# Kernel optimization log

Hardware: AMD Instinct MI355X
Metric: run time of the kernel (lower is better)

Reference implementation:

```python
import jax, jax.numpy as jnp
import numpy as np

B, C, H, W = 4, 256, 128, 128
D = 256            # attention hidden_dim (== C, so no output_proj)
HID = 1024         # mlp hidden = int(C * 4.0)
EPS = 1e-5


def setup_inputs() -> dict:
    key = jax.random.key(0)
    ks = jax.random.split(key, 16)
    s = 0.02
    return {
        "x": jax.random.normal(ks[0], (B, C, H, W), jnp.float32),
        "wq": jax.random.normal(ks[1], (C, D), jnp.float32) * s,
        "bq": jnp.zeros((D,), jnp.float32),
        "wk": jax.random.normal(ks[2], (C, D), jnp.float32) * s,
        "bk": jnp.zeros((D,), jnp.float32),
        "wv": jax.random.normal(ks[3], (C, D), jnp.float32) * s,
        "bv": jnp.zeros((D,), jnp.float32),
        "ln1_g": jnp.ones((C,), jnp.float32),
        "ln1_b": jnp.zeros((C,), jnp.float32),
        "ln2_g": jnp.ones((C,), jnp.float32),
        "ln2_b": jnp.zeros((C,), jnp.float32),
        "fc1_w": jax.random.normal(ks[4], (C, HID), jnp.float32) * s,
        "fc1_b": jnp.zeros((HID,), jnp.float32),
        "fc2_w": jax.random.normal(ks[5], (HID, C), jnp.float32) * s,
        "fc2_b": jnp.zeros((C,), jnp.float32),
    }


def _layernorm(x, g, b):
    m = jnp.mean(x, axis=-1, keepdims=True)
    v = jnp.mean(jnp.square(x - m), axis=-1, keepdims=True)
    return (x - m) * jax.lax.rsqrt(v + EPS) * g + b


def _neighborhoods(t):
    # t: [B,H,W,D] -> [B,H,W,9,D] 3x3 neighborhoods, zero-padded at borders
    tp = jnp.pad(t, ((0, 0), (1, 1), (1, 1), (0, 0)))
    h, w = t.shape[1], t.shape[2]
    return jnp.stack(
        [tp[:, dy:dy + h, dx:dx + w, :] for dy in range(3) for dx in range(3)],
        axis=3,
    )


def _valid_mask(h, w):
    # [H,W,9] bool: which of the 9 neighbors are inside the grid
    ys = jnp.arange(h)[:, None] * jnp.ones((1, w), jnp.int32)
    xs = jnp.arange(w)[None, :] * jnp.ones((h, 1), jnp.int32)
    top, bot = ys > 0, ys < h - 1
    lef, rig = xs > 0, xs < w - 1
    ones = jnp.ones((h, w), bool)
    return jnp.stack(
        [top & lef, top, top & rig, lef, ones, rig, bot & lef, bot, bot & rig],
        axis=-1,
    )


def reference(x, wq, bq, wk, bk, wv, bv, ln1_g, ln1_b, ln2_g, ln2_b,
              fc1_w, fc1_b, fc2_w, fc2_b):
    b_, c_, h_, w_ = x.shape
    xc = jnp.transpose(x, (0, 2, 3, 1))                    # [B,H,W,C]
    n1 = _layernorm(xc, ln1_g, ln1_b)
    q = n1 @ wq + bq                                       # [B,H,W,D]
    k = n1 @ wk + bk
    v = n1 @ wv + bv
    kn = _neighborhoods(k)                                  # [B,H,W,9,D]
    vn = _neighborhoods(v)
    scores = jnp.einsum('bhwd,bhwnd->bhwn', q, kn) / jnp.sqrt(jnp.float32(q.shape[-1]))
    mask = _valid_mask(h_, w_)                               # [H,W,9]
    scores = jnp.where(mask, scores, jnp.float32(-1e9))
    weights = jax.nn.softmax(scores, axis=-1)
    attn = jnp.einsum('bhwn,bhwnd->bhwd', weights, vn)       # [B,H,W,D]
    x1 = xc + attn                                           # residual 1
    n2 = _layernorm(x1, ln2_g, ln2_b)
    mlp = jax.nn.gelu(n2 @ fc1_w + fc1_b, approximate=False) @ fc2_w + fc2_b
    out = x1 + mlp
    return jnp.transpose(out, (0, 3, 1, 2))                  # [B,C,H,W]
```

## Files before the change

kernel.cpp:

```cpp
#include <hip/hip_runtime.h>
#include <hip/hip_bf16.h>
#include <math.h>

#define NPIX  65536
#define CCH   256
#define HWSZ  16384
#define WIDTH 128
#define HID   1024

typedef unsigned short u16;
typedef __bf16 bf16x8 __attribute__((ext_vector_type(8)));
typedef float  floatx4 __attribute__((ext_vector_type(4)));

__device__ __forceinline__ float bf2f(u16 u) {
  union { unsigned int i; float f; } c; c.i = ((unsigned int)u) << 16; return c.f;
}
__device__ __forceinline__ float bflo(unsigned int u) {
  union { unsigned int i; float f; } c; c.i = u << 16; return c.f;
}
__device__ __forceinline__ float bfhi(unsigned int u) {
  union { unsigned int i; float f; } c; c.i = u & 0xffff0000u; return c.f;
}
__device__ __forceinline__ u16 f2bf(float f) {
  union { float f; unsigned int i; } c; c.f = f;
  unsigned int x = c.i;
  x += 0x7fffu + ((x >> 16) & 1u);
  return (u16)(x >> 16);
}
__device__ __forceinline__ unsigned int packbf(float lo, float hi) {
  return ((unsigned int)f2bf(hi) << 16) | (unsigned int)f2bf(lo);
}
__device__ __forceinline__ float fast_rcp(float x) {
  float r; asm("v_rcp_f32 %0, %1" : "=v"(r) : "v"(x)); return r;
}
__device__ __forceinline__ float fast_exp2(float x) {
  float r; asm("v_exp_f32 %0, %1" : "=v"(r) : "v"(x)); return r;
}
__device__ __forceinline__ float gelu_fast(float x) {
  const float u = x * x;
  const float s = x * fmaf(0.1029432f, u, 2.3022082f);
  const float e = fast_exp2(-s);
  return x * fast_rcp(1.0f + e);
}

__device__ __forceinline__ void async16(const void* g, void* l) {
  __builtin_amdgcn_global_load_lds(
      (const __attribute__((address_space(1))) void*)g,
      (__attribute__((address_space(3))) void*)l, 16, 0, 0);
}

__global__ __launch_bounds__(256) void wfrag_kernel(
    const float* __restrict__ src, u16* __restrict__ dst, int N, int K) {
  const int tid = threadIdx.x;
  const int u = blockIdx.x * 4 + (tid >> 6);
  const int lane = tid & 63, quad = lane >> 4, l16 = lane & 15;
  const int K32 = K >> 5;
  const int g = u / K32, kb = u - g * K32;
  const int n = g * 16 + l16;
  const int k0 = kb * 32 + quad * 8;
  u16 tmp[8];
#pragma unroll
  for (int e = 0; e < 8; e++) tmp[e] = f2bf(src[(size_t)(k0 + e) * N + n]);
  *(bf16x8*)(dst + ((size_t)u * 64 + lane) * 8) = *(bf16x8*)tmp;
}

__global__ __launch_bounds__(256) void concat_bias_kernel(
    const float* __restrict__ bq, const float* __restrict__ bk,
    const float* __restrict__ bv, float* __restrict__ dst) {
  const int i = blockIdx.x * 256 + threadIdx.x;
  if (i < 256) dst[i] = bq[i];
  else if (i < 512) dst[i] = bk[i - 256];
  else if (i < 768) dst[i] = bv[i - 512];
}

__global__ __launch_bounds__(256) void ln1_kernel(
    const float* __restrict__ x, const float* __restrict__ g,
    const float* __restrict__ bb, u16* __restrict__ n1) {
  __shared__ float sx[32][257];
  __shared__ float sred[16][32];
  __shared__ float sm[32], sr[32];
  const int tx = threadIdx.x;
  const int p0 = blockIdx.x * 32;
  {
    const int pix = tx & 31, cpart = tx >> 5;
    const int p = p0 + pix;
    const int b = p >> 14, hw = p & (HWSZ - 1);
    const float* xb = x + ((size_t)b * CCH) * HWSZ + hw;
    float s = 0.f, s2 = 0.f;
#pragma unroll 4
    for (int i = 0; i < 32; i++) {
      const int c = cpart * 32 + i;
      const float v = xb[(size_t)c * HWSZ];
      sx[pix][c] = v;
      s += v; s2 += v * v;
    }
    sred[cpart][pix] = s; sred[8 + cpart][pix] = s2;
  }
  __syncthreads();
  if (tx < 32) {
    float s = 0.f, s2 = 0.f;
#pragma unroll
    for (int j = 0; j < 8; j++) { s += sred[j][tx]; s2 += sred[8 + j][tx]; }
    const float m = s * (1.0f / 256.0f);
    const float var = s2 * (1.0f / 256.0f) - m * m;
    sm[tx] = m; sr[tx] = rsqrtf(var + 1e-5f);
  }
  __syncthreads();
  const float gc = g[tx], bc = bb[tx];
#pragma unroll 4
  for (int i = 0; i < 32; i++) {
    const float v = (sx[i][tx] - sm[i]) * sr[i] * gc + bc;
    n1[(size_t)(p0 + i) * CCH + tx] = f2bf(v);
  }
}

__global__ __launch_bounds__(256) void res_ln2_kernel(
    const float* __restrict__ x, const u16* __restrict__ attn,
    const float* __restrict__ g, const float* __restrict__ bb,
    float* __restrict__ x1, u16* __restrict__ n2) {
  __shared__ float sx[32][257];
  __shared__ float sred[16][32];
  __shared__ float sm[32], sr[32];
  const int tx = threadIdx.x;
  const int p0 = blockIdx.x * 32;
  {
    const int pix = tx & 31, cpart = tx >> 5;
    const int p = p0 + pix;
    const int b = p >> 14, hw = p & (HWSZ - 1);
    const float* xb = x + ((size_t)b * CCH) * HWSZ + hw;
#pragma unroll 4
    for (int i = 0; i < 32; i++) {
      const int c = cpart * 32 + i;
      sx[pix][c] = xb[(size_t)c * HWSZ];
    }
  }
  __syncthreads();
#pragma unroll 4
  for (int i = 0; i < 32; i++) {
    const float v = sx[i][tx] + bf2f(attn[(size_t)(p0 + i) * CCH + tx]);
    sx[i][tx] = v;
    x1[(size_t)(p0 + i) * CCH + tx] = v;
  }
  __syncthreads();
  {
    const int pix = tx & 31, cpart = tx >> 5;
    float s = 0.f, s2 = 0.f;
#pragma unroll 4
    for (int i = 0; i < 32; i++) {
      const float v = sx[pix][cpart * 32 + i];
      s += v; s2 += v * v;
    }
    sred[cpart][pix] = s; sred[8 + cpart][pix] = s2;
  }
  __syncthreads();
  if (tx < 32) {
    float s = 0.f, s2 = 0.f;
#pragma unroll
    for (int j = 0; j < 8; j++) { s += sred[j][tx]; s2 += sred[8 + j][tx]; }
    const float m = s * (1.0f / 256.0f);
    const float var = s2 * (1.0f / 256.0f) - m * m;
    sm[tx] = m; sr[tx] = rsqrtf(var + 1e-5f);
  }
  __syncthreads();
  const float gc = g[tx], bc = bb[tx];
#pragma unroll 4
  for (int i = 0; i < 32; i++) {
    const float v = (sx[i][tx] - sm[i]) * sr[i] * gc + bc;
    n2[(size_t)(p0 + i) * CCH + tx] = f2bf(v);
  }
}

__global__ __launch_bounds__(256) void attn_kernel(
    const u16* __restrict__ qkv, u16* __restrict__ attn) {
  const int tid = threadIdx.x;
  const int wave = tid >> 6, lane = tid & 63;
  const int p = blockIdx.x * 4 + wave;
  const int hw = p & (HWSZ - 1);
  const int hh = hw >> 7, ww = hw & (WIDTH - 1);
  const u16* rowp = qkv + (size_t)p * 768 + lane * 4;
  const uint2 qr = *(const uint2*)rowp;
  const float qf0 = bflo(qr.x), qf1 = bfhi(qr.x);
  const float qf2 = bflo(qr.y), qf3 = bfhi(qr.y);
  float sc[9];
#pragma unroll
  for (int n = 0; n < 9; n++) {
    const int dy = n / 3 - 1, dx = n % 3 - 1;
    const int y = hh + dy, x2 = ww + dx;
    float s = -1e30f;
    if (y >= 0 && y < 128 && x2 >= 0 && x2 < 128) {
      const uint2 kr = *(const uint2*)(rowp + 256 + (dy * WIDTH + dx) * 768);
      float d = qf0 * bflo(kr.x) + qf1 * bfhi(kr.x)
              + qf2 * bflo(kr.y) + qf3 * bfhi(kr.y);
#pragma unroll
      for (int o = 32; o >= 1; o >>= 1) d += __shfl_xor(d, o, 64);
      s = d * 0.0625f;
    }
    sc[n] = s;
  }
  float mx = sc[0];
#pragma unroll
  for (int n = 1; n < 9; n++) mx = fmaxf(mx, sc[n]);
  float wgt[9], wsum = 0.f;
#pragma unroll
  for (int n = 0; n < 9; n++) { wgt[n] = __expf(sc[n] - mx); wsum += wgt[n]; }
  const float inv = 1.0f / wsum;
  float a0 = 0.f, a1 = 0.f, a2 = 0.f, a3 = 0.f;
#pragma unroll
  for (int n = 0; n < 9; n++) {
    const int dy = n / 3 - 1, dx = n % 3 - 1;
    const int y = hh + dy, x2 = ww + dx;
    if (y >= 0 && y < 128 && x2 >= 0 && x2 < 128) {
      const uint2 vr = *(const uint2*)(rowp + 512 + (dy * WIDTH + dx) * 768);
      const float wn = wgt[n] * inv;
      a0 += wn * bflo(vr.x); a1 += wn * bfhi(vr.x);
      a2 += wn * bflo(vr.y); a3 += wn * bfhi(vr.y);
    }
  }
  uint2 o;
  o.x = ((unsigned int)f2bf(a1) << 16) | (unsigned int)f2bf(a0);
  o.y = ((unsigned int)f2bf(a3) << 16) | (unsigned int)f2bf(a2);
  *(uint2*)(attn + (size_t)p * CCH + lane * 4) = o;
}

template <int NCH, int NST, int EPI>
__global__ __launch_bounds__(256, 3) void gemm_blds(
    const u16* __restrict__ A, const u16* __restrict__ wf,
    const float* __restrict__ bias, u16* __restrict__ outb) {
  __shared__ u16 sB[2][16384];
  const int tid  = threadIdx.x;
  const int wave = tid >> 6, lane = tid & 63;
  const int quad = lane >> 4, l16 = lane & 15;
  const int m0 = blockIdx.x * 128 + wave * 32;

  const u16* aRow = A + (size_t)(m0 + l16) * CCH + quad * 8;
  bf16x8 afr[2][8];
#pragma unroll
  for (int mi = 0; mi < 2; mi++)
#pragma unroll
    for (int ks = 0; ks < 8; ks++)
      afr[mi][ks] = *(const bf16x8*)(aRow + (size_t)mi * 16 * CCH + ks * 32);

  u16* rowPtr0 = outb + (size_t)(m0 + l16) * NST;
  u16* rowPtr1 = rowPtr0 + (size_t)16 * NST;

  auto stage = [&](int ch, int buf) {
    const u16* g = wf + (size_t)ch * 16384;
#pragma unroll
    for (int i = 0; i < 8; i++)
      async16(g + i * 2048 + tid * 8, &sB[buf][i * 2048 + tid * 8]);
  };

  stage(0, 0);
#pragma unroll 1
  for (int ch = 0; ch < NCH; ++ch) {
    if (ch == 0) asm volatile("s_waitcnt vmcnt(0)" ::: "memory");
    else         asm volatile("s_waitcnt vmcnt(8)" ::: "memory");
    __builtin_amdgcn_s_barrier();
    __builtin_amdgcn_sched_barrier(0);
    floatx4 bs4pre[4];
#pragma unroll
    for (int gi = 0; gi < 4; gi++)
      bs4pre[gi] = *(const floatx4*)&bias[ch * 64 + gi * 16 + quad * 4];
    if (ch + 1 < NCH) stage(ch + 1, (ch + 1) & 1);
    __builtin_amdgcn_sched_barrier(0);
    const u16* sb = sB[ch & 1];
    floatx4 acc[2][4];
#pragma unroll
    for (int mi = 0; mi < 2; mi++)
#pragma unroll
      for (int gi = 0; gi < 4; gi++) acc[mi][gi] = (floatx4){0.f, 0.f, 0.f, 0.f};
#pragma unroll
    for (int ks = 0; ks < 8; ks++) {
      bf16x8 bfr[4];
#pragma unroll
      for (int gi = 0; gi < 4; gi++)
        bfr[gi] = *(const bf16x8*)&sb[(gi * 8 + ks) * 512 + lane * 8];
#pragma unroll
      for (int mi = 0; mi < 2; mi++)
#pragma unroll
        for (int gi = 0; gi < 4; gi++)
          acc[mi][gi] = __builtin_amdgcn_mfma_f32_16x16x32_bf16(
              bfr[gi], afr[mi][ks], acc[mi][gi], 0, 0, 0);
    }
#pragma unroll
    for (int gi = 0; gi < 4; gi++) {
      const int colb = ch * 64 + gi * 16 + quad * 4;
      const floatx4 bs4 = bs4pre[gi];
#pragma unroll
      for (int mi = 0; mi < 2; mi++) {
        float v[4];
#pragma unroll
        for (int r = 0; r < 4; r++) {
          float val = acc[mi][gi][r] + bs4[r];
          if constexpr (EPI == 1) val = gelu_fast(val);
          v[r] = val;
        }
        uint2 w;
        w.x = packbf(v[0], v[1]);
        w.y = packbf(v[2], v[3]);
        *(uint2*)((mi == 0 ? rowPtr0 : rowPtr1) + colb) = w;
      }
    }
  }
}

__global__ __launch_bounds__(256, 2) void mlp_kernel(
    const u16* __restrict__ n2, const u16* __restrict__ f1F,
    const u16* __restrict__ f2F, const float* __restrict__ b1,
    const float* __restrict__ b2, const float* __restrict__ x1,
    float* __restrict__ out) {
  __shared__ u16 sW[2][16384];
  __shared__ __align__(16) u16 hx[4][16][72];
  const int tid  = threadIdx.x;
  const int wave = tid >> 6, lane = tid & 63;
  const int quad = lane >> 4, l16 = lane & 15;
  const int m0w = blockIdx.x * 64 + wave * 16;

  const u16* aRow = n2 + (size_t)(m0w + l16) * CCH + quad * 8;
  bf16x8 afr[8];
#pragma unroll
  for (int ks = 0; ks < 8; ks++)
    afr[ks] = *(const bf16x8*)(aRow + ks * 32);

  auto stageW1 = [&](int hc, int buf) {
    const u16* g = f1F + (size_t)hc * 16384;
#pragma unroll
    for (int i = 0; i < 8; i++)
      async16(g + i * 2048 + tid * 8, &sW[buf][i * 2048 + tid * 8]);
  };

  const u16* w2Base = f2F + lane * 8;

  floatx4 acc2[16];
#pragma unroll
  for (int gi2 = 0; gi2 < 16; gi2++) acc2[gi2] = (floatx4){0.f, 0.f, 0.f, 0.f};

  stageW1(0, 0);
#pragma unroll 1
  for (int hc = 0; hc < 16; ++hc) {
    __syncthreads();
    bf16x8 w2a[16];
#pragma unroll
    for (int gi2 = 0; gi2 < 16; gi2++)
      w2a[gi2] = *(const bf16x8*)(w2Base + (((size_t)gi2 * 32 + hc * 2) << 9));
    if (hc + 1 < 16) stageW1(hc + 1, (hc + 1) & 1);
    floatx4 bs1[4];
#pragma unroll
    for (int gi = 0; gi < 4; gi++)
      bs1[gi] = *(const floatx4*)&b1[hc * 64 + gi * 16 + quad * 4];
    const u16* sb = sW[hc & 1];
    floatx4 acc1[4];
#pragma unroll
    for (int gi = 0; gi < 4; gi++) acc1[gi] = (floatx4){0.f, 0.f, 0.f, 0.f};
#pragma unroll
    for (int ks = 0; ks < 8; ks++) {
      bf16x8 bfr[4];
#pragma unroll
      for (int gi = 0; gi < 4; gi++)
        bfr[gi] = *(const bf16x8*)&sb[(gi * 8 + ks) * 512 + lane * 8];
#pragma unroll
      for (int gi = 0; gi < 4; gi++)
        acc1[gi] = __builtin_amdgcn_mfma_f32_16x16x32_bf16(
            bfr[gi], afr[ks], acc1[gi], 0, 0, 0);
    }
#pragma unroll
    for (int gi = 0; gi < 4; gi++) {
      float v[4];
#pragma unroll
      for (int r = 0; r < 4; r++) v[r] = gelu_fast(acc1[gi][r] + bs1[gi][r]);
      uint2 w;
      w.x = packbf(v[0], v[1]);
      w.y = packbf(v[2], v[3]);
      *(uint2*)&hx[wave][l16][gi * 16 + quad * 4] = w;
    }
    bf16x8 hfrag[2];
#pragma unroll
    for (int ks2 = 0; ks2 < 2; ks2++)
      hfrag[ks2] = *(const bf16x8*)&hx[wave][l16][ks2 * 32 + quad * 8];
#pragma unroll
    for (int gi2 = 0; gi2 < 16; gi2++)
      acc2[gi2] = __builtin_amdgcn_mfma_f32_16x16x32_bf16(
          hfrag[0], w2a[gi2], acc2[gi2], 0, 0, 0);
#pragma unroll
    for (int gi2 = 0; gi2 < 16; gi2++) {
      const bf16x8 w2b = *(const bf16x8*)(w2Base + (((size_t)gi2 * 32 + hc * 2 + 1) << 9));
      acc2[gi2] = __builtin_amdgcn_mfma_f32_16x16x32_bf16(
          hfrag[1], w2b, acc2[gi2], 0, 0, 0);
    }
  }

#pragma unroll
  for (int gi2 = 0; gi2 < 16; gi2++) {
    const int col = gi2 * 16 + l16;
    const float bs = b2[col];
    const int row0 = m0w + quad * 4;
    floatx4 vv;
#pragma unroll
    for (int r = 0; r < 4; r++)
      vv[r] = acc2[gi2][r] + bs + x1[(size_t)(row0 + r) * CCH + col];
    *(floatx4*)&out[((size_t)((row0 >> 14) * CCH + col)) * HWSZ + (row0 & (HWSZ - 1))] = vv;
  }
}

extern "C" void kernel_launch(void* const* d_in, const int* in_sizes, int n_in,
                              void* d_out, int out_size, void* d_ws, size_t ws_size,
                              hipStream_t stream) {
  const float* x    = (const float*)d_in[0];
  const float* wq   = (const float*)d_in[1];
  const float* bq   = (const float*)d_in[2];
  const float* wk   = (const float*)d_in[3];
  const float* bk   = (const float*)d_in[4];
  const float* wv   = (const float*)d_in[5];
  const float* bv   = (const float*)d_in[6];
  const float* ln1g = (const float*)d_in[7];
  const float* ln1b = (const float*)d_in[8];
  const float* ln2g = (const float*)d_in[9];
  const float* ln2b = (const float*)d_in[10];
  const float* fc1w = (const float*)d_in[11];
  const float* fc1b = (const float*)d_in[12];
  const float* fc2w = (const float*)d_in[13];
  const float* fc2b = (const float*)d_in[14];
  float* out = (float*)d_out;

  char* ws = (char*)d_ws;
  const size_t MB = (size_t)1 << 20;
  float* x1   = (float*)(ws);
  u16* qkv    = (u16*)(ws + 64 * MB);
  u16* n1     = (u16*)(ws + 160 * MB);
  u16* attnb  = n1;
  u16* n2     = (u16*)(ws + 192 * MB);
  u16* wqkvF  = (u16*)(ws + 224 * MB);
  u16* f1F    = wqkvF + 768 * 256;
  u16* f2F    = f1F + 1024 * 256;
  float* bqkv = (float*)(f2F + 256 * 1024);

  dim3 blk(256);
  wfrag_kernel<<<dim3(32),  blk, 0, stream>>>(wq,   wqkvF,          256, 256);
  wfrag_kernel<<<dim3(32),  blk, 0, stream>>>(wk,   wqkvF + 65536,  256, 256);
  wfrag_kernel<<<dim3(32),  blk, 0, stream>>>(wv,   wqkvF + 131072, 256, 256);
  wfrag_kernel<<<dim3(128), blk, 0, stream>>>(fc1w, f1F, 1024, 256);
  wfrag_kernel<<<dim3(128), blk, 0, stream>>>(fc2w, f2F, 256, 1024);
  concat_bias_kernel<<<dim3(3), blk, 0, stream>>>(bq, bk, bv, bqkv);

  ln1_kernel<<<NPIX / 32, blk, 0, stream>>>(x, ln1g, ln1b, n1);

  gemm_blds<12, 768, 0><<<dim3(NPIX / 128), blk, 0, stream>>>(n1, wqkvF, bqkv, qkv);

  attn_kernel<<<NPIX / 4, blk, 0, stream>>>(qkv, attnb);

  res_ln2_kernel<<<NPIX / 32, blk, 0, stream>>>(x, attnb, ln2g, ln2b, x1, n2);

  mlp_kernel<<<dim3(NPIX / 64), blk, 0, stream>>>(n2, f1F, f2F, fc1b, fc2b, x1, out);
}
```

Before: 498.0 us.

## Split fc2 output columns across waves and share GELU hidden tile via LDS

New measurement: 399.6 us. -19.8%, faster.

```diff
diff --git a/kernel.cpp b/kernel.cpp
--- a/kernel.cpp
+++ b/kernel.cpp
@@ -310,11 +310,12 @@
     const float* __restrict__ b2, const float* __restrict__ x1,
     float* __restrict__ out) {
   __shared__ u16 sW[2][16384];
-  __shared__ __align__(16) u16 hx[4][16][72];
+  __shared__ __align__(16) u16 hL[64][72];
   const int tid  = threadIdx.x;
   const int wave = tid >> 6, lane = tid & 63;
   const int quad = lane >> 4, l16 = lane & 15;
-  const int m0w = blockIdx.x * 64 + wave * 16;
+  const int mblk = blockIdx.x * 64;
+  const int m0w  = mblk + wave * 16;
 
   const u16* aRow = n2 + (size_t)(m0w + l16) * CCH + quad * 8;
   bf16x8 afr[8];
@@ -329,21 +330,24 @@
       async16(g + i * 2048 + tid * 8, &sW[buf][i * 2048 + tid * 8]);
   };
 
-  const u16* w2Base = f2F + lane * 8;
-
-  floatx4 acc2[16];
-#pragma unroll
-  for (int gi2 = 0; gi2 < 16; gi2++) acc2[gi2] = (floatx4){0.f, 0.f, 0.f, 0.f};
+  const u16* w2Base = f2F + (((size_t)(wave * 4)) << 14) + lane * 8;
+
+  floatx4 acc2[4][4];
+#pragma unroll
+  for (int mi = 0; mi < 4; mi++)
+#pragma unroll
+    for (int gi = 0; gi < 4; gi++) acc2[mi][gi] = (floatx4){0.f, 0.f, 0.f, 0.f};
 
   stageW1(0, 0);
 #pragma unroll 1
   for (int hc = 0; hc < 16; ++hc) {
     __syncthreads();
-    bf16x8 w2a[16];
-#pragma unroll
-    for (int gi2 = 0; gi2 < 16; gi2++)
-      w2a[gi2] = *(const bf16x8*)(w2Base + (((size_t)gi2 * 32 + hc * 2) << 9));
-    if (hc + 1 < 16) stageW1(hc + 1, (hc + 1) & 1);
+    bf16x8 w2f[4][2];
+#pragma unroll
+    for (int gi = 0; gi < 4; gi++)
+#pragma unroll
+      for (int ks2 = 0; ks2 < 2; ks2++)
+        w2f[gi][ks2] = *(const bf16x8*)(w2Base + (((size_t)gi * 32 + hc * 2 + ks2) << 9));
     floatx4 bs1[4];
 #pragma unroll
     for (int gi = 0; gi < 4; gi++)
@@ -371,35 +375,35 @@
       uint2 w;
       w.x = packbf(v[0], v[1]);
       w.y = packbf(v[2], v[3]);
-      *(uint2*)&hx[wave][l16][gi * 16 + quad * 4] = w;
-    }
-    bf16x8 hfrag[2];
-#pragma unroll
-    for (int ks2 = 0; ks2 < 2; ks2++)
-      hfrag[ks2] = *(const bf16x8*)&hx[wave][l16][ks2 * 32 + quad * 8];
-#pragma unroll
-    for (int gi2 = 0; gi2 < 16; gi2++)
-      acc2[gi2] = __builtin_amdgcn_mfma_f32_16x16x32_bf16(
-          hfrag[0], w2a[gi2], acc2[gi2], 0, 0, 0);
-#pragma unroll
-    for (int gi2 = 0; gi2 < 16; gi2++) {
-      const bf16x8 w2b = *(const bf16x8*)(w2Base + (((size_t)gi2 * 32 + hc * 2 + 1) << 9));
-      acc2[gi2] = __builtin_amdgcn_mfma_f32_16x16x32_bf16(
-          hfrag[1], w2b, acc2[gi2], 0, 0, 0);
-    }
-  }
-
-#pragma unroll
-  for (int gi2 = 0; gi2 < 16; gi2++) {
-    const int col = gi2 * 16 + l16;
-    const float bs = b2[col];
-    const int row0 = m0w + quad * 4;
-    floatx4 vv;
-#pragma unroll
-    for (int r = 0; r < 4; r++)
-      vv[r] = acc2[gi2][r] + bs + x1[(size_t)(row0 + r) * CCH + col];
-    *(floatx4*)&out[((size_t)((row0 >> 14) * CCH + col)) * HWSZ + (row0 & (HWSZ - 1))] = vv;
-  }
+      *(uint2*)&hL[wave * 16 + l16][gi * 16 + quad * 4] = w;
+    }
+    __syncthreads();
+    if (hc + 1 < 16) stageW1(hc + 1, (hc + 1) & 1);
+#pragma unroll
+    for (int mi = 0; mi < 4; mi++)
+#pragma unroll
+      for (int ks2 = 0; ks2 < 2; ks2++) {
+        const bf16x8 hf = *(const bf16x8*)&hL[mi * 16 + l16][ks2 * 32 + quad * 8];
+#pragma unroll
+        for (int gi = 0; gi < 4; gi++)
+          acc2[mi][gi] = __builtin_amdgcn_mfma_f32_16x16x32_bf16(
+              hf, w2f[gi][ks2], acc2[mi][gi], 0, 0, 0);
+      }
+  }
+
+#pragma unroll
+  for (int mi = 0; mi < 4; mi++)
+#pragma unroll
+    for (int gi = 0; gi < 4; gi++) {
+      const int col = (wave * 4 + gi) * 16 + l16;
+      const float bs = b2[col];
+      const int row0 = mblk + mi * 16 + quad * 4;
+      floatx4 vv;
+#pragma unroll
+      for (int r = 0; r < 4; r++)
+        vv[r] = acc2[mi][gi][r] + bs + x1[(size_t)(row0 + r) * CCH + col];
+      *(floatx4*)&out[((size_t)((row0 >> 14) * CCH + col)) * HWSZ + (row0 & (HWSZ - 1))] = vv;
+    }
 }
 
 extern "C" void kernel_launch(void* const* d_in, const int* in_sizes, int n_in,
```
